# Optimization experiments

Hardware: AMD Instinct MI355X
Metric: run time of the kernel (lower is better)

## Reference

```python
import jax, jax.numpy as jnp
import numpy as np

B, T, C = 8, 2048, 1024
H, D = 16, 64  # n_heads, head_size; H*D == C


def setup_inputs() -> dict:
    key = jax.random.key(0)
    ks = jax.random.split(key, 6)
    s = 0.02
    x = jax.random.normal(ks[0], (B, T, C), dtype=jnp.float32)
    wq = jax.random.normal(ks[1], (H, C, D), dtype=jnp.float32) * s
    wk = jax.random.normal(ks[2], (H, C, D), dtype=jnp.float32) * s
    wv = jax.random.normal(ks[3], (H, C, D), dtype=jnp.float32) * s
    w_proj = jax.random.normal(ks[4], (H * D, C), dtype=jnp.float32) * s
    b_proj = jax.random.normal(ks[5], (C,), dtype=jnp.float32) * s
    return {"x": x, "wq": wq, "wk": wk, "wv": wv, "w_proj": w_proj, "b_proj": b_proj}


def reference(x, wq, wk, wv, w_proj, b_proj):
    Bq, Tq, Cq = x.shape
    # Batched per-head projections (original loops over heads with separate Linears)
    q = jnp.einsum('btc,hcd->bhtd', x, wq)
    k = jnp.einsum('btc,hcd->bhtd', x, wk)
    v = jnp.einsum('btc,hcd->bhtd', x, wv)
    # NOTE: source scales by C**-0.5 where C is the INPUT embed dim, not head_size
    wei = jnp.einsum('bhtd,bhsd->bhts', q, k) * (Cq ** -0.5)
    causal = jnp.tril(jnp.ones((Tq, Tq), dtype=bool))
    wei = jnp.where(causal, wei, jnp.float32(-jnp.inf))
    wei = jax.nn.softmax(wei, axis=-1)
    # dropout is identity in eval/reference mode
    out = jnp.einsum('bhts,bhsd->bhtd', wei, v)
    out = out.transpose(0, 2, 1, 3).reshape(Bq, Tq, H * D)  # concat over heads
    return out @ w_proj + b_proj
```

## Files before the change

### kernel.cpp

```cpp
#include <hip/hip_runtime.h>
#include <stdint.h>

#define DEV static __device__ __forceinline__

typedef __attribute__((ext_vector_type(8))) short bf16x8;
typedef __attribute__((ext_vector_type(4))) float f32x4;

constexpr int Bc = 8, Tc = 2048, Cc = 1024, Hc = 16, Dc = 64;

DEV ushort f2bf(float f) {
  union { float f; uint32_t u; } x{f};
  uint32_t r = (x.u + 0x7FFFu + ((x.u >> 16) & 1u)) >> 16;
  return (ushort)r;
}

DEV uint32_t cvt_pk_bf16(float a, float b) {
  uint32_t r;
  asm("v_cvt_pk_bf16_f32 %0, %1, %2" : "=v"(r) : "v"(a), "v"(b));
  return r;
}

DEV void gload16(const ushort* g, ushort* l) {
  __builtin_amdgcn_global_load_lds(
      (const __attribute__((address_space(1))) unsigned int*)g,
      (__attribute__((address_space(3))) unsigned int*)l, 16, 0, 0);
}

DEV f32x4 mfma16(bf16x8 a, bf16x8 b, f32x4 c) {
  return __builtin_amdgcn_mfma_f32_16x16x32_bf16(a, b, c, 0, 0, 0);
}

union B8 { bf16x8 v; uint4 u; };

__global__ __launch_bounds__(256) void k_conv_x(const float* __restrict__ x, ushort* __restrict__ xb) {
  int i = blockIdx.x * 256 + threadIdx.x;
  float4 v = ((const float4*)x)[i];
  ushort4 o = make_ushort4(f2bf(v.x), f2bf(v.y), f2bf(v.z), f2bf(v.w));
  ((ushort4*)xb)[i] = o;
}

__global__ __launch_bounds__(256) void k_conv_wqkv(const float* __restrict__ wq, const float* __restrict__ wk,
                                                   const float* __restrict__ wv, ushort* __restrict__ wt) {
  int i = blockIdx.x * 256 + threadIdx.x;
  int c = i & 1023;
  int n = i >> 10;
  int which = n >> 10;
  int rem = n & 1023;
  int h = rem >> 6, d = rem & 63;
  const float* src = which == 0 ? wq : (which == 1 ? wk : wv);
  float v = src[((size_t)h * 1024 + c) * 64 + d];
  if (which == 0) v *= 0.03125f * 1.44269504088896340736f;
  wt[i] = f2bf(v);
}

__global__ __launch_bounds__(256) void k_conv_wproj(const float* __restrict__ wp, ushort* __restrict__ wt) {
  int i = blockIdx.x * 256 + threadIdx.x;
  int n = i >> 10, k = i & 1023;
  wt[i] = f2bf(wp[(size_t)k * 1024 + n]);
}

DEV void gemm_main(const ushort* __restrict__ A, const ushort* __restrict__ BT,
                   int m0, int n0, int tid, ushort* lds_a, ushort* lds_b,
                   f32x4 (&acc)[4][4]) {
  const int lane = tid & 63, wid = tid >> 6;
  const int lr = lane & 15, lg = lane >> 4;
  const int wm = wid >> 1, wn = wid & 1;
  for (int kt = 0; kt < 16; ++kt) {
#pragma unroll
    for (int r = 0; r < 4; ++r) {
      int flat = r * 256 + tid;
      int row = flat >> 3, c8 = flat & 7;
      gload16(&A[(size_t)(m0 + row) * 1024 + kt * 64 + c8 * 8], &lds_a[flat * 8]);
      gload16(&BT[(size_t)(n0 + row) * 1024 + kt * 64 + c8 * 8], &lds_b[flat * 8]);
    }
    __syncthreads();
#pragma unroll
    for (int kc = 0; kc < 2; ++kc) {
      bf16x8 af[4], bfr[4];
#pragma unroll
      for (int mf = 0; mf < 4; ++mf)
        af[mf] = *(const bf16x8*)&lds_a[(wm * 64 + mf * 16 + lr) * 64 + kc * 32 + lg * 8];
#pragma unroll
      for (int nf = 0; nf < 4; ++nf)
        bfr[nf] = *(const bf16x8*)&lds_b[(wn * 64 + nf * 16 + lr) * 64 + kc * 32 + lg * 8];
      __builtin_amdgcn_s_setprio(1);
#pragma unroll
      for (int mf = 0; mf < 4; ++mf)
#pragma unroll
        for (int nf = 0; nf < 4; ++nf)
          acc[mf][nf] = mfma16(af[mf], bfr[nf], acc[mf][nf]);
      __builtin_amdgcn_s_setprio(0);
    }
    __syncthreads();
  }
}

__global__ __launch_bounds__(256) void k_gemm_qkv(const ushort* __restrict__ xb, const ushort* __restrict__ wt,
                                                  ushort* __restrict__ qws, ushort* __restrict__ kws,
                                                  ushort* __restrict__ vws) {
  __shared__ ushort lds_a[128 * 64];
  __shared__ ushort lds_b[128 * 64];
  const int tid = threadIdx.x;
  const int m0 = blockIdx.y * 128, n0 = blockIdx.x * 128;
  f32x4 acc[4][4];
  f32x4 z = {0.f, 0.f, 0.f, 0.f};
  for (int i = 0; i < 4; ++i) for (int j = 0; j < 4; ++j) acc[i][j] = z;
  gemm_main(xb, wt, m0, n0, tid, lds_a, lds_b, acc);
  const int lane = tid & 63, wid = tid >> 6;
  const int lr = lane & 15, lg = lane >> 4;
  const int wm = wid >> 1, wn = wid & 1;
#pragma unroll
  for (int mf = 0; mf < 4; ++mf)
#pragma unroll
    for (int nf = 0; nf < 4; ++nf)
#pragma unroll
      for (int r = 0; r < 4; ++r) {
        int m = m0 + wm * 64 + mf * 16 + lg * 4 + r;
        int n = n0 + wn * 64 + nf * 16 + lr;
        int which = n >> 10, rem = n & 1023;
        int h = rem >> 6, d = rem & 63;
        int b = m >> 11, t = m & 2047;
        ushort* dst = which == 0 ? qws : (which == 1 ? kws : vws);
        dst[((size_t)(b * Hc + h) * Tc + t) * 64 + d] = f2bf(acc[mf][nf][r]);
      }
}

__global__ __launch_bounds__(256) void k_vtrans(const ushort* __restrict__ v, ushort* __restrict__ vt) {
  __shared__ ushort lds[64][68];
  const int t0 = blockIdx.x * 64;
  const int bh = blockIdx.y;
  const int tid = threadIdx.x;
  const ushort* src = v + (size_t)bh * Tc * 64;
  ushort* dst = vt + (size_t)bh * 64 * Tc;
#pragma unroll
  for (int j = 0; j < 4; ++j) {
    int flat = j * 256 + tid;
    int row = flat >> 4, cg = flat & 15;
    ushort4 x = *(const ushort4*)&src[(size_t)(t0 + row) * 64 + cg * 4];
    lds[row][cg * 4 + 0] = x.x; lds[row][cg * 4 + 1] = x.y;
    lds[row][cg * 4 + 2] = x.z; lds[row][cg * 4 + 3] = x.w;
  }
  __syncthreads();
#pragma unroll
  for (int j = 0; j < 4; ++j) {
    int flat = j * 256 + tid;
    int d = flat >> 4, tg = flat & 15;
    ushort4 x = make_ushort4(lds[tg * 4 + 0][d], lds[tg * 4 + 1][d], lds[tg * 4 + 2][d], lds[tg * 4 + 3][d]);
    *(ushort4*)&dst[(size_t)d * Tc + t0 + tg * 4] = x;
  }
}

DEV int swz(int row, int bcol) { return row * 128 + (bcol ^ ((row & 7) << 4)); }

__global__ __launch_bounds__(256) void k_attn(const ushort* __restrict__ qws, const ushort* __restrict__ kws,
                                              const ushort* __restrict__ vtws, ushort* __restrict__ att) {
  const int id = blockIdx.x;
  const int xcd = id & 7, slot = id >> 3;
  const int bh = (xcd << 4) + (slot >> 3);
  const int qi = slot & 7;
  const int tid = threadIdx.x, lane = tid & 63, wid = tid >> 6;
  const int lr = lane & 15, lg = lane >> 4;

  __shared__ __align__(16) ushort lds_k[2 * 64 * 64];
  __shared__ __align__(16) ushort lds_v[2 * 64 * 64];

  const ushort* qbase = qws + (size_t)bh * Tc * 64;
  const ushort* kbase = kws + (size_t)bh * Tc * 64;
  const ushort* vtbase = vtws + (size_t)bh * 64 * Tc;
  const int b = bh >> 4, h = bh & 15;
  const f32x4 z = {0.f, 0.f, 0.f, 0.f};

  for (int pass = 0; pass < 2; ++pass) {
    const int qb = pass == 0 ? qi : 15 - qi;
    const int q0 = qb * 128;
    const int ntiles = 2 * qb + 2;
    const int qrow = q0 + wid * 32;
    const int qgmax = qrow + 31;

    bf16x8 qa[2][2];
#pragma unroll
    for (int qf = 0; qf < 2; ++qf)
#pragma unroll
      for (int kc = 0; kc < 2; ++kc)
        qa[qf][kc] = *(const bf16x8*)&qbase[(size_t)(qrow + qf * 16 + lr) * 64 + kc * 32 + lg * 8];

    f32x4 o[2][4];
    float m_[2], l_[2];
#pragma unroll
    for (int qf = 0; qf < 2; ++qf) {
#pragma unroll
      for (int df = 0; df < 4; ++df) o[qf][df] = z;
      m_[qf] = -1e30f; l_[qf] = 0.f;
    }

    __syncthreads();

    int4 kreg[2], vreg[2];
#pragma unroll
    for (int r = 0; r < 2; ++r) {
      int flat = r * 256 + tid;
      int row = flat >> 3, c8 = flat & 7;
      kreg[r] = *(const int4*)&kbase[(size_t)row * 64 + c8 * 8];
      vreg[r] = *(const int4*)&vtbase[(size_t)row * Tc + c8 * 8];
    }

    for (int it = 0; it < ntiles; ++it) {
      ushort* ldsK = lds_k + (it & 1) * 4096;
      ushort* ldsV = lds_v + (it & 1) * 4096;
#pragma unroll
      for (int r = 0; r < 2; ++r) {
        int flat = r * 256 + tid;
        int row = flat >> 3, c8 = flat & 7;
        *(int4*)((char*)ldsK + swz(row, c8 * 16)) = kreg[r];
        *(int4*)((char*)ldsV + swz(row, c8 * 16)) = vreg[r];
      }
      if (it + 1 < ntiles) {
        const int s0n = (it + 1) * 64;
#pragma unroll
        for (int r = 0; r < 2; ++r) {
          int flat = r * 256 + tid;
          int row = flat >> 3, c8 = flat & 7;
          kreg[r] = *(const int4*)&kbase[(size_t)(s0n + row) * 64 + c8 * 8];
          vreg[r] = *(const int4*)&vtbase[(size_t)row * Tc + s0n + c8 * 8];
        }
      }
      __syncthreads();

      const int s0 = it * 64;
      if (s0 > qgmax) continue;

      f32x4 s[4][2];
#pragma unroll
      for (int sf = 0; sf < 4; ++sf)
#pragma unroll
        for (int qf = 0; qf < 2; ++qf) s[sf][qf] = z;
#pragma unroll
      for (int kc = 0; kc < 2; ++kc) {
        bf16x8 kf[4];
#pragma unroll
        for (int sf = 0; sf < 4; ++sf)
          kf[sf] = *(const bf16x8*)((const char*)ldsK + swz(sf * 16 + lr, kc * 64 + lg * 16));
        __builtin_amdgcn_s_setprio(1);
#pragma unroll
        for (int sf = 0; sf < 4; ++sf)
#pragma unroll
          for (int qf = 0; qf < 2; ++qf)
            s[sf][qf] = mfma16(kf[sf], qa[qf][kc], s[sf][qf]);
        __builtin_amdgcn_s_setprio(0);
      }

      if (s0 + 63 > qrow) {
#pragma unroll
        for (int sf = 0; sf < 4; ++sf)
#pragma unroll
          for (int qf = 0; qf < 2; ++qf)
#pragma unroll
            for (int r = 0; r < 4; ++r) {
              int sg = s0 + sf * 16 + lg * 4 + r;
              int qg = qrow + qf * 16 + lr;
              if (sg > qg) s[sf][qf][r] = -1e30f;
            }
      }

      float sc[2];
      bool defer[2];
#pragma unroll
      for (int qf = 0; qf < 2; ++qf) {
        float t0_ = fmaxf(fmaxf(s[0][qf][0], s[0][qf][1]), fmaxf(s[0][qf][2], s[0][qf][3]));
        float t1_ = fmaxf(fmaxf(s[1][qf][0], s[1][qf][1]), fmaxf(s[1][qf][2], s[1][qf][3]));
        float t2_ = fmaxf(fmaxf(s[2][qf][0], s[2][qf][1]), fmaxf(s[2][qf][2], s[2][qf][3]));
        float t3_ = fmaxf(fmaxf(s[3][qf][0], s[3][qf][1]), fmaxf(s[3][qf][2], s[3][qf][3]));
        float t = fmaxf(fmaxf(t0_, t1_), fmaxf(t2_, t3_));
        t = fmaxf(t, __shfl_xor(t, 16));
        t = fmaxf(t, __shfl_xor(t, 32));
        defer[qf] = __all(t <= m_[qf] + 11.54f) != 0;
        float mnew = defer[qf] ? m_[qf] : fmaxf(m_[qf], t);
        sc[qf] = defer[qf] ? 1.f : exp2f(m_[qf] - mnew);
        m_[qf] = mnew;
        float sum = 0.f;
#pragma unroll
        for (int sf = 0; sf < 4; ++sf)
#pragma unroll
          for (int r = 0; r < 4; ++r) {
            float p = exp2f(s[sf][qf][r] - mnew);
            s[sf][qf][r] = p;
            sum += p;
          }
        sum += __shfl_xor(sum, 16);
        sum += __shfl_xor(sum, 32);
        l_[qf] = l_[qf] * sc[qf] + sum;
      }
#pragma unroll
      for (int qf = 0; qf < 2; ++qf)
        if (!defer[qf]) {
#pragma unroll
          for (int r = 0; r < 4; ++r) {
            float scR = __shfl(sc[qf], ((lane >> 4) << 2) + r);
#pragma unroll
            for (int df = 0; df < 4; ++df) o[qf][df][r] *= scR;
          }
        }

      uint32_t pk_[4][2][2];
#pragma unroll
      for (int sf = 0; sf < 4; ++sf)
#pragma unroll
        for (int qf = 0; qf < 2; ++qf) {
          pk_[sf][qf][0] = cvt_pk_bf16(s[sf][qf][0], s[sf][qf][1]);
          pk_[sf][qf][1] = cvt_pk_bf16(s[sf][qf][2], s[sf][qf][3]);
        }

#pragma unroll
      for (int kc = 0; kc < 2; ++kc) {
        B8 vf[4];
#pragma unroll
        for (int df = 0; df < 4; ++df) {
          uint2 lo = *(const uint2*)((const char*)ldsV + swz(df * 16 + lr, kc * 64 + lg * 8));
          uint2 hi = *(const uint2*)((const char*)ldsV + swz(df * 16 + lr, kc * 64 + 32 + lg * 8));
          vf[df].u = make_uint4(lo.x, lo.y, hi.x, hi.y);
        }
        B8 pf[2];
#pragma unroll
        for (int qf = 0; qf < 2; ++qf)
          pf[qf].u = make_uint4(pk_[2 * kc][qf][0], pk_[2 * kc][qf][1],
                                pk_[2 * kc + 1][qf][0], pk_[2 * kc + 1][qf][1]);
        __builtin_amdgcn_s_setprio(1);
#pragma unroll
        for (int qf = 0; qf < 2; ++qf)
#pragma unroll
          for (int df = 0; df < 4; ++df)
            o[qf][df] = mfma16(pf[qf].v, vf[df].v, o[qf][df]);
        __builtin_amdgcn_s_setprio(0);
      }
    }

#pragma unroll
    for (int qf = 0; qf < 2; ++qf)
#pragma unroll
      for (int r = 0; r < 4; ++r) {
        float lR = __shfl(l_[qf], ((lane >> 4) << 2) + r);
        float inv = 1.f / lR;
        int qg = qrow + qf * 16 + lg * 4 + r;
#pragma unroll
        for (int df = 0; df < 4; ++df) {
          int d = df * 16 + lr;
          att[(size_t)(b * Tc + qg) * 1024 + h * 64 + d] = f2bf(o[qf][df][r] * inv);
        }
      }
  }
}

__global__ __launch_bounds__(256) void k_gemm_proj(const ushort* __restrict__ attb, const ushort* __restrict__ wt,
                                                   const float* __restrict__ bias, float* __restrict__ out) {
  __shared__ ushort lds_a[128 * 64];
  __shared__ ushort lds_b[128 * 64];
  const int tid = threadIdx.x;
  const int m0 = blockIdx.y * 128, n0 = blockIdx.x * 128;
  f32x4 acc[4][4];
  f32x4 z = {0.f, 0.f, 0.f, 0.f};
  for (int i = 0; i < 4; ++i) for (int j = 0; j < 4; ++j) acc[i][j] = z;
  gemm_main(attb, wt, m0, n0, tid, lds_a, lds_b, acc);
  const int lane = tid & 63, wid = tid >> 6;
  const int lr = lane & 15, lg = lane >> 4;
  const int wm = wid >> 1, wn = wid & 1;
#pragma unroll
  for (int mf = 0; mf < 4; ++mf)
#pragma unroll
    for (int nf = 0; nf < 4; ++nf)
#pragma unroll
      for (int r = 0; r < 4; ++r) {
        int m = m0 + wm * 64 + mf * 16 + lg * 4 + r;
        int n = n0 + wn * 64 + nf * 16 + lr;
        out[(size_t)m * 1024 + n] = acc[mf][nf][r] + bias[n];
      }
}

extern "C" void kernel_launch(void* const* d_in, const int* in_sizes, int n_in,
                              void* d_out, int out_size, void* d_ws, size_t ws_size,
                              hipStream_t stream) {
  const float* x  = (const float*)d_in[0];
  const float* wq = (const float*)d_in[1];
  const float* wk = (const float*)d_in[2];
  const float* wv = (const float*)d_in[3];
  const float* wp = (const float*)d_in[4];
  const float* bp = (const float*)d_in[5];
  float* out = (float*)d_out;

  char* ws = (char*)d_ws;
  size_t off = 0;
  auto alloc = [&](size_t bytes) { char* p = ws + off; off += (bytes + 255) & ~255ull; return p; };
  ushort* xb   = (ushort*)alloc(16384ull * 1024 * 2);
  ushort* wqkv = (ushort*)alloc(3072ull * 1024 * 2);
  ushort* wpt  = (ushort*)alloc(1024ull * 1024 * 2);
  ushort* qws  = (ushort*)alloc(16384ull * 1024 * 2);
  ushort* kws  = (ushort*)alloc(16384ull * 1024 * 2);
  ushort* vws  = (ushort*)alloc(16384ull * 1024 * 2);
  ushort* vtws = (ushort*)alloc(16384ull * 1024 * 2);
  ushort* attb = xb;

  k_conv_x<<<16384, 256, 0, stream>>>(x, xb);
  k_conv_wqkv<<<12288, 256, 0, stream>>>(wq, wk, wv, wqkv);
  k_conv_wproj<<<4096, 256, 0, stream>>>(wp, wpt);
  k_gemm_qkv<<<dim3(24, 128), 256, 0, stream>>>(xb, wqkv, qws, kws, vws);
  k_vtrans<<<dim3(32, 128), 256, 0, stream>>>(vws, vtws);
  k_attn<<<1024, 256, 0, stream>>>(qws, kws, vtws, attb);
  k_gemm_proj<<<dim3(8, 128), 256, 0, stream>>>(attb, wpt, bp, out);
}
```

Measured before the change: 538.4 us.

## Use direct global-to-LDS loads, MFMA row sums, and max3 in attention

Replaces the register-staged K/V prefetch with global_load_lds asynchronous copies into the double-buffered LDS, with the XOR swizzle applied on the source column. This removes the VGPR staging and the explicit LDS stores. The softmax row sum is now accumulated by an extra MFMA against a ones vector instead of scalar adds and cross-lane shuffles. The row max uses v_max3, and launch bounds request 4 blocks per CU. Risks include extra MFMA work per tile, missing waits on the async loads before the barrier, and register pressure under the new occupancy bound.

After: 652.0 us. 21.1% more time.

```diff
diff --git a/kernel.cpp b/kernel.cpp
--- a/kernel.cpp
+++ b/kernel.cpp
@@ -17,6 +17,12 @@
 DEV uint32_t cvt_pk_bf16(float a, float b) {
   uint32_t r;
   asm("v_cvt_pk_bf16_f32 %0, %1, %2" : "=v"(r) : "v"(a), "v"(b));
+  return r;
+}
+
+DEV float max3f(float a, float b, float c) {
+  float r;
+  asm("v_max3_f32 %0, %1, %2, %3" : "=v"(r) : "v"(a), "v"(b), "v"(c));
   return r;
 }
 
@@ -152,8 +158,8 @@
 
 DEV int swz(int row, int bcol) { return row * 128 + (bcol ^ ((row & 7) << 4)); }
 
-__global__ __launch_bounds__(256) void k_attn(const ushort* __restrict__ qws, const ushort* __restrict__ kws,
-                                              const ushort* __restrict__ vtws, ushort* __restrict__ att) {
+__global__ __launch_bounds__(256, 4) void k_attn(const ushort* __restrict__ qws, const ushort* __restrict__ kws,
+                                                 const ushort* __restrict__ vtws, ushort* __restrict__ att) {
   const int id = blockIdx.x;
   const int xcd = id & 7, slot = id >> 3;
   const int bh = (xcd << 4) + (slot >> 3);
@@ -170,6 +176,21 @@
   const int b = bh >> 4, h = bh & 15;
   const f32x4 z = {0.f, 0.f, 0.f, 0.f};
 
+  int rowA[2], colA[2];
+#pragma unroll
+  for (int r = 0; r < 2; ++r) {
+    int flat = r * 256 + tid;
+    int row = flat >> 3, c8 = flat & 7;
+    rowA[r] = row;
+    colA[r] = 8 * (c8 ^ (row & 7));
+  }
+
+  B8 onesf;
+  {
+    uint32_t pp = lr == 0 ? 0x3F803F80u : 0u;
+    onesf.u = make_uint4(pp, pp, pp, pp);
+  }
+
   for (int pass = 0; pass < 2; ++pass) {
     const int qb = pass == 0 ? qi : 15 - qi;
     const int q0 = qb * 128;
@@ -185,46 +206,38 @@
         qa[qf][kc] = *(const bf16x8*)&qbase[(size_t)(qrow + qf * 16 + lr) * 64 + kc * 32 + lg * 8];
 
     f32x4 o[2][4];
-    float m_[2], l_[2];
+    f32x4 lac[2];
+    float m_[2];
 #pragma unroll
     for (int qf = 0; qf < 2; ++qf) {
 #pragma unroll
       for (int df = 0; df < 4; ++df) o[qf][df] = z;
-      m_[qf] = -1e30f; l_[qf] = 0.f;
+      lac[qf] = z;
+      m_[qf] = -1e30f;
     }
 
     __syncthreads();
 
-    int4 kreg[2], vreg[2];
 #pragma unroll
     for (int r = 0; r < 2; ++r) {
-      int flat = r * 256 + tid;
-      int row = flat >> 3, c8 = flat & 7;
-      kreg[r] = *(const int4*)&kbase[(size_t)row * 64 + c8 * 8];
-      vreg[r] = *(const int4*)&vtbase[(size_t)row * Tc + c8 * 8];
+      gload16(&kbase[(size_t)rowA[r] * 64 + colA[r]], &lds_k[(r * 256 + tid) * 8]);
+      gload16(&vtbase[(size_t)rowA[r] * Tc + colA[r]], &lds_v[(r * 256 + tid) * 8]);
     }
 
     for (int it = 0; it < ntiles; ++it) {
-      ushort* ldsK = lds_k + (it & 1) * 4096;
-      ushort* ldsV = lds_v + (it & 1) * 4096;
-#pragma unroll
-      for (int r = 0; r < 2; ++r) {
-        int flat = r * 256 + tid;
-        int row = flat >> 3, c8 = flat & 7;
-        *(int4*)((char*)ldsK + swz(row, c8 * 16)) = kreg[r];
-        *(int4*)((char*)ldsV + swz(row, c8 * 16)) = vreg[r];
-      }
+      __syncthreads();
+      const ushort* ldsK = lds_k + (it & 1) * 4096;
+      const ushort* ldsV = lds_v + (it & 1) * 4096;
       if (it + 1 < ntiles) {
         const int s0n = (it + 1) * 64;
+        ushort* dK = lds_k + ((it + 1) & 1) * 4096;
+        ushort* dV = lds_v + ((it + 1) & 1) * 4096;
 #pragma unroll
         for (int r = 0; r < 2; ++r) {
-          int flat = r * 256 + tid;
-          int row = flat >> 3, c8 = flat & 7;
-          kreg[r] = *(const int4*)&kbase[(size_t)(s0n + row) * 64 + c8 * 8];
-          vreg[r] = *(const int4*)&vtbase[(size_t)row * Tc + s0n + c8 * 8];
-        }
-      }
-      __syncthreads();
+          gload16(&kbase[(size_t)(s0n + rowA[r]) * 64 + colA[r]], &dK[(r * 256 + tid) * 8]);
+          gload16(&vtbase[(size_t)rowA[r] * Tc + s0n + colA[r]], &dV[(r * 256 + tid) * 8]);
+        }
+      }
 
       const int s0 = it * 64;
       if (s0 > qgmax) continue;
@@ -266,29 +279,23 @@
       bool defer[2];
 #pragma unroll
       for (int qf = 0; qf < 2; ++qf) {
-        float t0_ = fmaxf(fmaxf(s[0][qf][0], s[0][qf][1]), fmaxf(s[0][qf][2], s[0][qf][3]));
-        float t1_ = fmaxf(fmaxf(s[1][qf][0], s[1][qf][1]), fmaxf(s[1][qf][2], s[1][qf][3]));
-        float t2_ = fmaxf(fmaxf(s[2][qf][0], s[2][qf][1]), fmaxf(s[2][qf][2], s[2][qf][3]));
-        float t3_ = fmaxf(fmaxf(s[3][qf][0], s[3][qf][1]), fmaxf(s[3][qf][2], s[3][qf][3]));
-        float t = fmaxf(fmaxf(t0_, t1_), fmaxf(t2_, t3_));
+        float a0 = max3f(s[0][qf][0], s[0][qf][1], s[0][qf][2]);
+        float a1 = max3f(s[0][qf][3], s[1][qf][0], s[1][qf][1]);
+        float a2 = max3f(s[1][qf][2], s[1][qf][3], s[2][qf][0]);
+        float a3 = max3f(s[2][qf][1], s[2][qf][2], s[2][qf][3]);
+        float a4 = max3f(s[3][qf][0], s[3][qf][1], s[3][qf][2]);
+        float t = max3f(max3f(a0, a1, a2), a3, fmaxf(a4, s[3][qf][3]));
         t = fmaxf(t, __shfl_xor(t, 16));
         t = fmaxf(t, __shfl_xor(t, 32));
         defer[qf] = __all(t <= m_[qf] + 11.54f) != 0;
         float mnew = defer[qf] ? m_[qf] : fmaxf(m_[qf], t);
         sc[qf] = defer[qf] ? 1.f : exp2f(m_[qf] - mnew);
         m_[qf] = mnew;
-        float sum = 0.f;
 #pragma unroll
         for (int sf = 0; sf < 4; ++sf)
 #pragma unroll
-          for (int r = 0; r < 4; ++r) {
-            float p = exp2f(s[sf][qf][r] - mnew);
-            s[sf][qf][r] = p;
-            sum += p;
-          }
-        sum += __shfl_xor(sum, 16);
-        sum += __shfl_xor(sum, 32);
-        l_[qf] = l_[qf] * sc[qf] + sum;
+          for (int r = 0; r < 4; ++r)
+            s[sf][qf][r] = exp2f(s[sf][qf][r] - mnew);
       }
 #pragma unroll
       for (int qf = 0; qf < 2; ++qf)
@@ -298,6 +305,7 @@
             float scR = __shfl(sc[qf], ((lane >> 4) << 2) + r);
 #pragma unroll
             for (int df = 0; df < 4; ++df) o[qf][df][r] *= scR;
+            lac[qf][r] *= scR;
           }
         }
 
@@ -326,10 +334,12 @@
                                 pk_[2 * kc + 1][qf][0], pk_[2 * kc + 1][qf][1]);
         __builtin_amdgcn_s_setprio(1);
 #pragma unroll
-        for (int qf = 0; qf < 2; ++qf)
+        for (int qf = 0; qf < 2; ++qf) {
 #pragma unroll
           for (int df = 0; df < 4; ++df)
             o[qf][df] = mfma16(pf[qf].v, vf[df].v, o[qf][df]);
+          lac[qf] = mfma16(pf[qf].v, onesf.v, lac[qf]);
+        }
         __builtin_amdgcn_s_setprio(0);
       }
     }
@@ -338,7 +348,7 @@
     for (int qf = 0; qf < 2; ++qf)
 #pragma unroll
       for (int r = 0; r < 4; ++r) {
-        float lR = __shfl(l_[qf], ((lane >> 4) << 2) + r);
+        float lR = __shfl(lac[qf][r], lg << 4);
         float inv = 1.f / lR;
         int qg = qrow + qf * 16 + lg * 4 + r;
 #pragma unroll
```
